# Performance work log

Measured on AMD Instinct MI355X. Metric: run time of the kernel, lower is better.

The kernel has to match this reference:

```python
import jax, jax.numpy as jnp
import numpy as np
from jax import lax

B, C, H, W = 2, 64, 128, 128
F_SCALE, STRIDE = 2, 2
F = F_SCALE * STRIDE            # pixel-unshuffle factor = 4
CK = C // 16                    # attention channel dim = 4
SCALE_DIM = C // F_SCALE        # softmax scale uses embed_size//f_scale = 32


def setup_inputs() -> dict:
    key = jax.random.key(0)
    ks = jax.random.split(key, 16)
    g = lambda i, shape, s=0.05: jax.random.normal(ks[i], shape, jnp.float32) * s
    return {
        "x":   jax.random.normal(ks[0], (B, C, H, W), jnp.float32),
        # conv1 = Sequential(1x1 C->CK, 1x1 CK->CK)
        "w1a": g(1, (CK, C)), "b1a": g(2, (CK,)),
        "w1b": g(3, (CK, CK)), "b1b": g(4, (CK,)),
        # wqk parameter (torch.randn, std 1)
        "wqk": jax.random.normal(ks[5], (CK, CK), jnp.float32),
        # conv2: 1x1 CK->C ; conv: 1x1 C->C
        "w2":  g(6, (C, CK)), "b2": g(7, (C,)),
        "wc":  g(8, (C, C)), "bc": g(9, (C,)),
        # FF (GridSANaive): 1x1 C->C/4, 3x3 dilated C/4->C/4, 1x1 C/4->C
        "wf1": g(10, (C // 4, C)), "bf1": g(11, (C // 4,)),
        "wf2": g(12, (C // 4, C // 4, 3, 3)), "bf2": g(13, (C // 4,)),
        "wf3": g(14, (C, C // 4)), "bf3": g(15, (C,)),
    }


def conv1x1(x, w, b):
    return jnp.einsum('bchw,oc->bohw', x, w) + b[None, :, None, None]


def grid_attention(x, wqk):
    b, c, h, w = x.shape
    sh = h // 2
    x = jnp.pad(x, ((0, 0), (0, 0), (sh, 0), (0, 0)))      # Shift2d pad (top)
    # F.layer_norm over last 3 dims, no affine, eps=1e-5
    mu = jnp.mean(x, axis=(1, 2, 3), keepdims=True)
    var = jnp.var(x, axis=(1, 2, 3), keepdims=True)
    xx = (x - mu) / jnp.sqrt(var + 1e-5)
    hh, ww = xx.shape[2], xx.shape[3]
    ph, pw = (F - hh % F) % F, (F - ww % F) % F
    xx = jnp.pad(xx, ((0, 0), (0, 0), (0, ph), (0, pw)))
    gh, gw = (hh + ph) // F, (ww + pw) // F
    # pixel_unshuffle: channel layout (c, fy, fx)
    xx = xx.reshape(b, c, gh, F, gw, F).transpose(0, 1, 3, 5, 2, 4)
    xx = xx.reshape(b, c * F * F, gh, gw)
    # rearrange 'b (f c) h w -> (b f) c h w', f=F*F (mixes layout, as in original)
    xx = xx.reshape(b * F * F, c, gh, gw)
    L = gh * gw
    tok = xx.transpose(0, 2, 3, 1).reshape(b * F * F, L, c)   # (bg, L, c)
    qk = tok @ wqk
    qk = qk / (jnp.linalg.norm(qk, axis=-1, keepdims=True) + 1e-8)
    attn = (jnp.einsum('blk,bmk->blm', qk, qk) + 1.0) / (SCALE_DIM ** 0.5)
    attn = jax.nn.softmax(attn, axis=-1)
    out = jnp.einsum('blm,bmc->blc', attn, tok)
    out = out.reshape(b * F * F, gh, gw, c).transpose(0, 3, 1, 2)
    out = out.reshape(b, F * F * c, gh, gw)
    # pixel_shuffle: channel layout (fy, fx, c)
    out = out.reshape(b, F, F, c, gh, gw).transpose(0, 3, 4, 1, 5, 2)
    out = out.reshape(b, c, gh * F, gw * F)
    out = out[:, :, :hh, :ww]                               # undo shuffle pad
    return out[:, :, :-sh, :] if sh > 0 else out            # Shift2d crop (bottom)


def ff(x, wf1, bf1, wf2, bf2, wf3, bf3):
    h1 = jax.nn.relu(conv1x1(x, wf1, bf1))
    k = 1 + (STRIDE // 2) * 2   # ShiftConv2d offset for 3x3, dilation=STRIDE
    hp = jnp.pad(h1, ((0, 0), (0, 0), (k, 0), (0, 0)))
    h2 = lax.conv_general_dilated(
        hp, wf2, (1, 1), ((STRIDE, STRIDE), (STRIDE, STRIDE)),
        rhs_dilation=(STRIDE, STRIDE),
        dimension_numbers=('NCHW', 'OIHW', 'NCHW'))
    h2 = jax.nn.relu((h2 + bf2[None, :, None, None])[:, :, :-k, :])
    return conv1x1(h2, wf3, bf3)


def reference(x, w1a, b1a, w1b, b1b, wqk, w2, b2, wc, bc,
              wf1, bf1, wf2, bf2, wf3, bf3):
    a = conv1x1(conv1x1(x, w1a, b1a), w1b, b1b)
    att = grid_attention(a, wqk)
    y = x + conv1x1(conv1x1(att, w2, b2), wc, bc)
    return y + ff(y, wf1, bf1, wf2, bf2, wf3, bf3)
```

## Files before the change

kernel.cpp:

```cpp
#include <hip/hip_runtime.h>
#include <math.h>

#define CHW  (64*16384)
#define ATT_SCALE 0.17677669529663687f

__global__ __launch_bounds__(256) void k1_a_stats(
    const float* __restrict__ x, const float* __restrict__ w1a,
    const float* __restrict__ b1a, const float* __restrict__ w1b,
    const float* __restrict__ b1b, float* __restrict__ a,
    float* __restrict__ statsbuf) {
  __shared__ float sA[256];
  __shared__ float sb1[4];
  __shared__ float pc[4][4][256];
  __shared__ float rs[64], rq[64];
  int tid = threadIdx.x;
  {
    int o = tid >> 6, c = tid & 63;
    float s = 0.f;
    #pragma unroll
    for (int k = 0; k < 4; ++k) s += w1b[o*4+k] * w1a[k*64+c];
    sA[tid] = s;
  }
  if (tid < 4) {
    float s = b1b[tid];
    #pragma unroll
    for (int k = 0; k < 4; ++k) s += w1b[tid*4+k] * b1a[k];
    sb1[tid] = s;
  }
  __syncthreads();
  int quad = tid & 15, cg = tid >> 4;
  int gq = blockIdx.x * 16 + quad;
  int bb = gq >> 12;
  int px0 = (gq & 4095) * 4;
  const float* xp = x + bb*CHW + (cg*4)*16384 + px0;
  float4 acc[4];
  #pragma unroll
  for (int o = 0; o < 4; ++o) acc[o] = make_float4(0.f,0.f,0.f,0.f);
  #pragma unroll
  for (int cc = 0; cc < 4; ++cc) {
    float4 xv = *(const float4*)(xp + cc*16384);
    int c = cg*4 + cc;
    #pragma unroll
    for (int o = 0; o < 4; ++o) {
      float w = sA[o*64+c];
      acc[o].x += w*xv.x; acc[o].y += w*xv.y; acc[o].z += w*xv.z; acc[o].w += w*xv.w;
    }
  }
  #pragma unroll
  for (int o = 0; o < 4; ++o) {
    pc[0][o][tid] = acc[o].x; pc[1][o][tid] = acc[o].y;
    pc[2][o][tid] = acc[o].z; pc[3][o][tid] = acc[o].w;
  }
  __syncthreads();
  if (tid < 64) {
    int q2 = tid & 15, o = tid >> 4;
    float sx=0.f, sy=0.f, sz=0.f, sw=0.f;
    #pragma unroll
    for (int g2 = 0; g2 < 16; ++g2) {
      int idx = g2*16 + q2;
      sx += pc[0][o][idx]; sy += pc[1][o][idx];
      sz += pc[2][o][idx]; sw += pc[3][o][idx];
    }
    float bv = sb1[o];
    sx += bv; sy += bv; sz += bv; sw += bv;
    int gq2 = blockIdx.x*16 + q2;
    int b2 = gq2 >> 12; int p0 = (gq2 & 4095)*4;
    *(float4*)(a + b2*4*16384 + o*16384 + p0) = make_float4(sx,sy,sz,sw);
    rs[tid] = sx+sy+sz+sw;
    rq[tid] = sx*sx+sy*sy+sz*sz+sw*sw;
  }
  __syncthreads();
  for (int s2 = 32; s2; s2 >>= 1) {
    if (tid < s2) { rs[tid] += rs[tid+s2]; rq[tid] += rq[tid+s2]; }
    __syncthreads();
  }
  if (tid == 0) { statsbuf[blockIdx.x*2] = rs[0]; statsbuf[blockIdx.x*2+1] = rq[0]; }
}

__device__ __forceinline__ float poly_exp(float d) {
  return 1.f + d*(1.f + d*(0.5f + d*(0.16666667f + d*0.04166667f)));
}
__global__ __launch_bounds__(512) void k3_attn(
    const float* __restrict__ a, const float* __restrict__ statsbuf,
    const float* __restrict__ wqk, float* __restrict__ att) {
  __shared__ float4 kq[1024];
  __shared__ float4 kt[1024];
  __shared__ float red[16][5][128];
  __shared__ float sred[8];
  int tid = threadIdx.x;
  int g = blockIdx.x >> 3, qb = blockIdx.x & 7;
  int b = g >> 4, u = (g >> 2) & 3, v = g & 3;

  if (tid < 256) {
    float2 p = ((const float2*)statsbuf)[b*256 + tid];
    float vs = p.x, vq = p.y;
    #pragma unroll
    for (int off = 32; off; off >>= 1) {
      vs += __shfl_down(vs, off); vq += __shfl_down(vq, off);
    }
    if ((tid & 63) == 0) { sred[tid>>6] = vs; sred[4 + (tid>>6)] = vq; }
  }
  __syncthreads();
  float mu  = (sred[0]+sred[1]+sred[2]+sred[3]) * (1.f/98304.f);
  float var = (sred[4]+sred[5]+sred[6]+sred[7]) * (1.f/98304.f) - mu*mu;
  float rsig = rsqrtf(var + 1e-5f);

  const float* ap = a + (b*4+u)*16384;
  for (int m = tid; m < 1024; m += 512) {
    int t = 512 + m;
    int i = t >> 5, j = m & 31;
    float4 tv = *(const float4*)(ap + (i*4 + v - 64)*128 + j*4);
    tv.x = (tv.x-mu)*rsig; tv.y = (tv.y-mu)*rsig;
    tv.z = (tv.z-mu)*rsig; tv.w = (tv.w-mu)*rsig;
    float q0 = tv.x*wqk[0] + tv.y*wqk[4] + tv.z*wqk[8]  + tv.w*wqk[12];
    float q1 = tv.x*wqk[1] + tv.y*wqk[5] + tv.z*wqk[9]  + tv.w*wqk[13];
    float q2 = tv.x*wqk[2] + tv.y*wqk[6] + tv.z*wqk[10] + tv.w*wqk[14];
    float q3 = tv.x*wqk[3] + tv.y*wqk[7] + tv.z*wqk[11] + tv.w*wqk[15];
    float inv = 1.f / (sqrtf(q0*q0 + q1*q1 + q2*q2 + q3*q3) + 1e-8f);
    kq[m] = make_float4(q0*inv, q1*inv, q2*inv, q3*inv);
    kt[m] = tv;
  }
  float z = -mu*rsig;
  float4 t0tv = make_float4(z, z, z, z);
  float p0 = z*(wqk[0] + wqk[4] + wqk[8]  + wqk[12]);
  float p1 = z*(wqk[1] + wqk[5] + wqk[9]  + wqk[13]);
  float p2 = z*(wqk[2] + wqk[6] + wqk[10] + wqk[14]);
  float p3 = z*(wqk[3] + wqk[7] + wqk[11] + wqk[15]);
  float inv0 = 1.f / (sqrtf(p0*p0 + p1*p1 + p2*p2 + p3*p3) + 1e-8f);
  float4 t0qk = make_float4(p0*inv0, p1*inv0, p2*inv0, p3*inv0);
  __syncthreads();

  if (qb >= 4) {
    int qi = tid & 31, s = tid >> 5;
    int t0 = (qb - 4)*128 + qi*4;
    float4 q[4];
    #pragma unroll
    for (int j = 0; j < 4; ++j) {
      float4 vq = kq[t0 + j];
      q[j] = make_float4(vq.x*ATT_SCALE, vq.y*ATT_SCALE, vq.z*ATT_SCALE, vq.w*ATT_SCALE);
    }
    float den[4] = {0.f,0.f,0.f,0.f};
    float4 ov[4];
    #pragma unroll
    for (int j = 0; j < 4; ++j) ov[j] = make_float4(0.f,0.f,0.f,0.f);
    if (s == 0) {
      #pragma unroll
      for (int j = 0; j < 4; ++j) {
        float d = q[j].x*t0qk.x + q[j].y*t0qk.y + q[j].z*t0qk.z + q[j].w*t0qk.w;
        float e = 512.f * poly_exp(d);
        den[j] += e;
        ov[j].x += e*t0tv.x; ov[j].y += e*t0tv.y; ov[j].z += e*t0tv.z; ov[j].w += e*t0tv.w;
      }
    }
    int m0 = s * 64;
    #pragma unroll 2
    for (int m = m0; m < m0 + 64; ++m) {
      float4 kk = kq[m];
      float4 tv = kt[m];
      #pragma unroll
      for (int j = 0; j < 4; ++j) {
        float d = q[j].x*kk.x + q[j].y*kk.y + q[j].z*kk.z + q[j].w*kk.w;
        float e = poly_exp(d);
        den[j] += e;
        ov[j].x += e*tv.x; ov[j].y += e*tv.y; ov[j].z += e*tv.z; ov[j].w += e*tv.w;
      }
    }
    #pragma unroll
    for (int j = 0; j < 4; ++j) {
      int key = j*32 + qi;
      red[s][0][key] = den[j];
      red[s][1][key] = ov[j].x; red[s][2][key] = ov[j].y;
      red[s][3][key] = ov[j].z; red[s][4][key] = ov[j].w;
    }
    __syncthreads();
    if (tid < 128) {
      int qi_r = tid & 31, j_r = tid >> 5;
      float dsum=0.f, ox=0.f, oy=0.f, oz=0.f, ow=0.f;
      #pragma unroll
      for (int ss = 0; ss < 16; ++ss) {
        dsum += red[ss][0][tid];
        ox += red[ss][1][tid]; oy += red[ss][2][tid];
        oz += red[ss][3][tid]; ow += red[ss][4][tid];
      }
      float inv = 1.f / dsum;
      int t = qb*128 + qi_r*4 + j_r;
      int i = t >> 5, j = t & 31;
      float* ap2 = att + b*4*16384 + (i*4+u)*128 + (j*4+v);
      ap2[0]     = ox*inv;
      ap2[16384] = oy*inv;
      ap2[32768] = oz*inv;
      ap2[49152] = ow*inv;
    }
  } else {
    float4 qs = make_float4(t0qk.x*ATT_SCALE, t0qk.y*ATT_SCALE,
                            t0qk.z*ATT_SCALE, t0qk.w*ATT_SCALE);
    float den = 0.f; float4 ov = make_float4(0.f,0.f,0.f,0.f);
    #pragma unroll
    for (int mm = 0; mm < 2; ++mm) {
      int m = tid*2 + mm;
      float4 kk = kq[m];
      float4 tv = kt[m];
      float d = qs.x*kk.x + qs.y*kk.y + qs.z*kk.z + qs.w*kk.w;
      float e = poly_exp(d);
      den += e;
      ov.x += e*tv.x; ov.y += e*tv.y; ov.z += e*tv.z; ov.w += e*tv.w;
    }
    if (tid == 0) {
      float d = qs.x*t0qk.x + qs.y*t0qk.y + qs.z*t0qk.z + qs.w*t0qk.w;
      float e = 512.f * poly_exp(d);
      den += e;
      ov.x += e*t0tv.x; ov.y += e*t0tv.y; ov.z += e*t0tv.z; ov.w += e*t0tv.w;
    }
    float* sc = &red[0][0][0];
    sc[tid]        = den;
    sc[512 + tid]  = ov.x;
    sc[1024 + tid] = ov.y;
    sc[1536 + tid] = ov.z;
    sc[2048 + tid] = ov.w;
    __syncthreads();
    for (int s2 = 256; s2; s2 >>= 1) {
      if (tid < s2) {
        sc[tid]        += sc[tid + s2];
        sc[512 + tid]  += sc[512 + tid + s2];
        sc[1024 + tid] += sc[1024 + tid + s2];
        sc[1536 + tid] += sc[1536 + tid + s2];
        sc[2048 + tid] += sc[2048 + tid + s2];
      }
      __syncthreads();
    }
    float invd = 1.f / sc[0];
    float res0 = sc[512]*invd, res1 = sc[1024]*invd,
          res2 = sc[1536]*invd, res3 = sc[2048]*invd;
    int comp = tid >> 7, tloc = tid & 127;
    int t = qb*128 + tloc;
    int i = t >> 5, j = t & 31;
    float val = (comp == 0) ? res0 : (comp == 1) ? res1 : (comp == 2) ? res2 : res3;
    att[b*4*16384 + comp*16384 + (i*4+u)*128 + (j*4+v)] = val;
  }
}

__global__ __launch_bounds__(512) void k4_y_h1(
    const float* __restrict__ x, const float* __restrict__ att,
    const float* __restrict__ w2p, const float* __restrict__ b2p,
    const float* __restrict__ wcp, const float* __restrict__ bcp,
    const float* __restrict__ wf1, const float* __restrict__ bf1,
    float* __restrict__ yout, float* __restrict__ h1) {
  __shared__ float sWf[64][4];
  __shared__ float sbf[64];
  __shared__ float sw1[1024];
  __shared__ float sb1[16];
  __shared__ float4 satt[4][32];
  __shared__ float4 ylds[64][32];
  int tid = threadIdx.x;
  if (tid < 256) {
    int o = tid >> 2, k = tid & 3;
    float s = 0.f;
    for (int c = 0; c < 64; ++c) s += wcp[o*64+c] * w2p[c*4+k];
    sWf[o][k] = s;
  }
  if (tid < 64) {
    float s = bcp[tid];
    for (int c = 0; c < 64; ++c) s += wcp[tid*64+c] * b2p[c];
    sbf[tid] = s;
  }
  for (int i = tid; i < 1024; i += 512) sw1[i] = wf1[i];
  if (tid < 16) sb1[tid] = bf1[tid];
  int quad = tid & 31, og = tid >> 5;
  int gq = blockIdx.x*32 + quad;
  int bb = gq >> 12; int px0 = (gq & 4095)*4;
  if (tid < 128) {
    int k = tid >> 5, q2 = tid & 31;
    int gq2 = blockIdx.x*32 + q2;
    int b2i = gq2 >> 12; int p0 = (gq2 & 4095)*4;
    satt[k][q2] = *(const float4*)(att + b2i*4*16384 + k*16384 + p0);
  }
  __syncthreads();
  float4 a0 = satt[0][quad], a1 = satt[1][quad], a2 = satt[2][quad], a3 = satt[3][quad];
  const float* xp = x + bb*CHW + px0;
  float* yp = yout + bb*CHW + px0;
  #pragma unroll
  for (int cc = 0; cc < 4; ++cc) {
    int c = og*4 + cc;
    float4 xv = *(const float4*)(xp + c*16384);
    float w0 = sWf[c][0], w1 = sWf[c][1], w2v = sWf[c][2], w3 = sWf[c][3];
    float bv = sbf[c];
    float4 yv;
    yv.x = xv.x + w0*a0.x + w1*a1.x + w2v*a2.x + w3*a3.x + bv;
    yv.y = xv.y + w0*a0.y + w1*a1.y + w2v*a2.y + w3*a3.y + bv;
    yv.z = xv.z + w0*a0.z + w1*a1.z + w2v*a2.z + w3*a3.z + bv;
    yv.w = xv.w + w0*a0.w + w1*a1.w + w2v*a2.w + w3*a3.w + bv;
    *(float4*)(yp + c*16384) = yv;
    ylds[c][quad] = yv;
  }
  __syncthreads();
  float bv = sb1[og];
  float4 acc = make_float4(bv, bv, bv, bv);
  #pragma unroll 8
  for (int c = 0; c < 64; ++c) {
    float4 yv = ylds[c][quad];
    float wa = sw1[og*64+c];
    acc.x += wa*yv.x; acc.y += wa*yv.y; acc.z += wa*yv.z; acc.w += wa*yv.w;
  }
  acc.x = fmaxf(acc.x,0.f); acc.y = fmaxf(acc.y,0.f);
  acc.z = fmaxf(acc.z,0.f); acc.w = fmaxf(acc.w,0.f);
  *(float4*)(h1 + bb*16*16384 + og*16384 + px0) = acc;
}

__global__ __launch_bounds__(512) void k6_ff_out(
    const float* __restrict__ h1, const float* __restrict__ wf2,
    const float* __restrict__ bf2, const float* __restrict__ wf3,
    const float* __restrict__ bf3, float* yo) {
  __shared__ float sbuf[16][3][136];
  __shared__ float h2buf[128][21];
  int tid = threadIdx.x;
  int bb = blockIdx.x >> 7, h = blockIdx.x & 127;
  for (int idx = tid; idx < 16*3*136; idx += 512) {
    int c = idx / (3*136);
    int r = (idx / 136) % 3;
    int col = idx % 136;
    int row = h - 5 + 2*r;
    int w = col - 4;
    float v = 0.f;
    if (row >= 0 && w >= 0 && w < 128)
      v = h1[bb*16*16384 + c*16384 + row*128 + w];
    sbuf[c][r][col] = v;
  }
  __syncthreads();
  int w = tid & 127;
  int g = __builtin_amdgcn_readfirstlane(tid >> 7);
  float acc[4];
  #pragma unroll
  for (int o = 0; o < 4; ++o) acc[o] = bf2[g*4+o];
  #pragma unroll 4
  for (int c = 0; c < 16; ++c) {
    #pragma unroll
    for (int r = 0; r < 3; ++r) {
      float tm2 = sbuf[c][r][w+2];
      float t00 = sbuf[c][r][w+4];
      float tp2 = sbuf[c][r][w+6];
      #pragma unroll
      for (int o = 0; o < 4; ++o) {
        const float* wp = wf2 + (((g*4+o)*16 + c)*3 + r)*3;
        acc[o] += wp[0]*tm2 + wp[1]*t00 + wp[2]*tp2;
      }
    }
  }
  #pragma unroll
  for (int o = 0; o < 4; ++o) h2buf[w][g*4+o] = fmaxf(acc[o], 0.f);
  __syncthreads();
  float hv[16];
  #pragma unroll
  for (int k = 0; k < 16; ++k) hv[k] = h2buf[w][k];
  float* ybase = yo + bb*CHW + h*128 + w;
  #pragma unroll 4
  for (int oc = 0; oc < 16; ++oc) {
    int o = g*16 + oc;
    float sv = bf3[o] + ybase[o*16384];
    #pragma unroll
    for (int k = 0; k < 16; ++k) sv += wf3[o*16+k]*hv[k];
    ybase[o*16384] = sv;
  }
}

extern "C" void kernel_launch(void* const* d_in, const int* in_sizes, int n_in,
                              void* d_out, int out_size, void* d_ws, size_t ws_size,
                              hipStream_t stream) {
  (void)in_sizes; (void)n_in; (void)out_size; (void)ws_size;
  const float* x   = (const float*)d_in[0];
  const float* w1a = (const float*)d_in[1];
  const float* b1a = (const float*)d_in[2];
  const float* w1b = (const float*)d_in[3];
  const float* b1b = (const float*)d_in[4];
  const float* wqk = (const float*)d_in[5];
  const float* w2  = (const float*)d_in[6];
  const float* b2  = (const float*)d_in[7];
  const float* wc  = (const float*)d_in[8];
  const float* bc  = (const float*)d_in[9];
  const float* wf1 = (const float*)d_in[10];
  const float* bf1 = (const float*)d_in[11];
  const float* wf2 = (const float*)d_in[12];
  const float* bf2 = (const float*)d_in[13];
  const float* wf3 = (const float*)d_in[14];
  const float* bf3 = (const float*)d_in[15];

  float* ws = (float*)d_ws;
  float*  a_    = ws;
  float*  stats = ws + 131072;
  float*  att   = ws + 525312;
  float*  h1    = ws + 656384;
  float*  y     = (float*)d_out;

  k1_a_stats<<<512, 256, 0, stream>>>(x, w1a, b1a, w1b, b1b, a_, stats);
  k3_attn   <<<256, 512, 0, stream>>>(a_, stats, wqk, att);
  k4_y_h1   <<<256, 512, 0, stream>>>(x, att, w2, b2, wc, bc, wf1, bf1, y, h1);
  k6_ff_out <<<256, 512, 0, stream>>>(h1, wf2, bf2, wf3, bf3, y);
}
```

Baseline: 130.9 us.

## Fuse y/h1 computation with FF conv into a single per-row kernel

Merges the residual-y and h1 kernel with the dilated-conv FF output kernel. Each block handles one output row and recomputes y and h1 for the three dilated input rows plus its own row in shared memory. This removes the global h1 buffer, the y write/read round trip and one kernel launch. In exchange it does about three times the y/h1 work and adds extra block barriers. The block index is also remapped across batch and rows.

```diff
diff --git a/kernel.cpp b/kernel.cpp
--- a/kernel.cpp
+++ b/kernel.cpp
@@ -239,19 +239,26 @@
   }
 }
 
-__global__ __launch_bounds__(512) void k4_y_h1(
+__global__ __launch_bounds__(512) void k46_row(
     const float* __restrict__ x, const float* __restrict__ att,
     const float* __restrict__ w2p, const float* __restrict__ b2p,
     const float* __restrict__ wcp, const float* __restrict__ bcp,
     const float* __restrict__ wf1, const float* __restrict__ bf1,
-    float* __restrict__ yout, float* __restrict__ h1) {
+    const float* __restrict__ wf2, const float* __restrict__ bf2,
+    const float* __restrict__ wf3, const float* __restrict__ bf3,
+    float* __restrict__ yo) {
   __shared__ float sWf[64][4];
   __shared__ float sbf[64];
   __shared__ float sw1[1024];
   __shared__ float sb1[16];
   __shared__ float4 satt[4][32];
   __shared__ float4 ylds[64][32];
+  __shared__ float sbuf[16][3][136];
+  __shared__ float h2buf[128][21];
   int tid = threadIdx.x;
+  int lid = (blockIdx.x & 7) * 32 + (blockIdx.x >> 3);
+  int bb = lid >> 7, h = lid & 127;
+
   if (tid < 256) {
     int o = tid >> 2, k = tid & 3;
     float s = 0.f;
@@ -265,67 +272,56 @@
   }
   for (int i = tid; i < 1024; i += 512) sw1[i] = wf1[i];
   if (tid < 16) sb1[tid] = bf1[tid];
+  for (int idx = tid; idx < 16*3*136; idx += 512) (&sbuf[0][0][0])[idx] = 0.f;
+
   int quad = tid & 31, og = tid >> 5;
-  int gq = blockIdx.x*32 + quad;
-  int bb = gq >> 12; int px0 = (gq & 4095)*4;
-  if (tid < 128) {
-    int k = tid >> 5, q2 = tid & 31;
-    int gq2 = blockIdx.x*32 + q2;
-    int b2i = gq2 >> 12; int p0 = (gq2 & 4095)*4;
-    satt[k][q2] = *(const float4*)(att + b2i*4*16384 + k*16384 + p0);
-  }
-  __syncthreads();
-  float4 a0 = satt[0][quad], a1 = satt[1][quad], a2 = satt[2][quad], a3 = satt[3][quad];
-  const float* xp = x + bb*CHW + px0;
-  float* yp = yout + bb*CHW + px0;
-  #pragma unroll
-  for (int cc = 0; cc < 4; ++cc) {
-    int c = og*4 + cc;
-    float4 xv = *(const float4*)(xp + c*16384);
-    float w0 = sWf[c][0], w1 = sWf[c][1], w2v = sWf[c][2], w3 = sWf[c][3];
-    float bv = sbf[c];
-    float4 yv;
-    yv.x = xv.x + w0*a0.x + w1*a1.x + w2v*a2.x + w3*a3.x + bv;
-    yv.y = xv.y + w0*a0.y + w1*a1.y + w2v*a2.y + w3*a3.y + bv;
-    yv.z = xv.z + w0*a0.z + w1*a1.z + w2v*a2.z + w3*a3.z + bv;
-    yv.w = xv.w + w0*a0.w + w1*a1.w + w2v*a2.w + w3*a3.w + bv;
-    *(float4*)(yp + c*16384) = yv;
-    ylds[c][quad] = yv;
-  }
-  __syncthreads();
-  float bv = sb1[og];
-  float4 acc = make_float4(bv, bv, bv, bv);
-  #pragma unroll 8
-  for (int c = 0; c < 64; ++c) {
-    float4 yv = ylds[c][quad];
-    float wa = sw1[og*64+c];
-    acc.x += wa*yv.x; acc.y += wa*yv.y; acc.z += wa*yv.z; acc.w += wa*yv.w;
-  }
-  acc.x = fmaxf(acc.x,0.f); acc.y = fmaxf(acc.y,0.f);
-  acc.z = fmaxf(acc.z,0.f); acc.w = fmaxf(acc.w,0.f);
-  *(float4*)(h1 + bb*16*16384 + og*16384 + px0) = acc;
-}
-
-__global__ __launch_bounds__(512) void k6_ff_out(
-    const float* __restrict__ h1, const float* __restrict__ wf2,
-    const float* __restrict__ bf2, const float* __restrict__ wf3,
-    const float* __restrict__ bf3, float* yo) {
-  __shared__ float sbuf[16][3][136];
-  __shared__ float h2buf[128][21];
-  int tid = threadIdx.x;
-  int bb = blockIdx.x >> 7, h = blockIdx.x & 127;
-  for (int idx = tid; idx < 16*3*136; idx += 512) {
-    int c = idx / (3*136);
-    int r = (idx / 136) % 3;
-    int col = idx % 136;
-    int row = h - 5 + 2*r;
-    int w = col - 4;
-    float v = 0.f;
-    if (row >= 0 && w >= 0 && w < 128)
-      v = h1[bb*16*16384 + c*16384 + row*128 + w];
-    sbuf[c][r][col] = v;
-  }
-  __syncthreads();
+  #pragma unroll 1
+  for (int ri = 0; ri < 4; ++ri) {
+    int row = (ri == 3) ? h : (h - 5 + 2*ri);
+    bool valid = (row >= 0);
+    __syncthreads();
+    if (valid && tid < 128) {
+      int k = tid >> 5, q2 = tid & 31;
+      satt[k][q2] = *(const float4*)(att + bb*4*16384 + k*16384 + row*128 + q2*4);
+    }
+    __syncthreads();
+    if (valid) {
+      float4 a0 = satt[0][quad], a1 = satt[1][quad],
+             a2 = satt[2][quad], a3 = satt[3][quad];
+      const float* xp = x + bb*CHW + row*128 + quad*4;
+      #pragma unroll
+      for (int cc = 0; cc < 4; ++cc) {
+        int c = og*4 + cc;
+        float4 xv = *(const float4*)(xp + c*16384);
+        float w0 = sWf[c][0], w1 = sWf[c][1], w2v = sWf[c][2], w3 = sWf[c][3];
+        float bv = sbf[c];
+        float4 yv;
+        yv.x = xv.x + w0*a0.x + w1*a1.x + w2v*a2.x + w3*a3.x + bv;
+        yv.y = xv.y + w0*a0.y + w1*a1.y + w2v*a2.y + w3*a3.y + bv;
+        yv.z = xv.z + w0*a0.z + w1*a1.z + w2v*a2.z + w3*a3.z + bv;
+        yv.w = xv.w + w0*a0.w + w1*a1.w + w2v*a2.w + w3*a3.w + bv;
+        ylds[c][quad] = yv;
+      }
+    }
+    __syncthreads();
+    if (valid && ri < 3) {
+      float bv = sb1[og];
+      float4 acc = make_float4(bv, bv, bv, bv);
+      #pragma unroll 8
+      for (int c = 0; c < 64; ++c) {
+        float4 yv = ylds[c][quad];
+        float wa = sw1[og*64+c];
+        acc.x += wa*yv.x; acc.y += wa*yv.y; acc.z += wa*yv.z; acc.w += wa*yv.w;
+      }
+      int col = 4 + quad*4;
+      sbuf[og][ri][col]   = fmaxf(acc.x, 0.f);
+      sbuf[og][ri][col+1] = fmaxf(acc.y, 0.f);
+      sbuf[og][ri][col+2] = fmaxf(acc.z, 0.f);
+      sbuf[og][ri][col+3] = fmaxf(acc.w, 0.f);
+    }
+  }
+  __syncthreads();
+
   int w = tid & 127;
   int g = __builtin_amdgcn_readfirstlane(tid >> 7);
   float acc[4];
@@ -351,11 +347,12 @@
   float hv[16];
   #pragma unroll
   for (int k = 0; k < 16; ++k) hv[k] = h2buf[w][k];
+  const float* yrow = (const float*)ylds;
   float* ybase = yo + bb*CHW + h*128 + w;
   #pragma unroll 4
   for (int oc = 0; oc < 16; ++oc) {
     int o = g*16 + oc;
-    float sv = bf3[o] + ybase[o*16384];
+    float sv = bf3[o] + yrow[o*128 + w];
     #pragma unroll
     for (int k = 0; k < 16; ++k) sv += wf3[o*16+k]*hv[k];
     ybase[o*16384] = sv;
@@ -387,11 +384,9 @@
   float*  a_    = ws;
   float*  stats = ws + 131072;
   float*  att   = ws + 525312;
-  float*  h1    = ws + 656384;
-  float*  y     = (float*)d_out;
 
   k1_a_stats<<<512, 256, 0, stream>>>(x, w1a, b1a, w1b, b1b, a_, stats);
   k3_attn   <<<256, 512, 0, stream>>>(a_, stats, wqk, att);
-  k4_y_h1   <<<256, 512, 0, stream>>>(x, att, w2, b2, wc, bc, wf1, bf1, y, h1);
-  k6_ff_out <<<256, 512, 0, stream>>>(h1, wf2, bf2, wf3, bf3, y);
-}
+  k46_row   <<<256, 512, 0, stream>>>(x, att, w2, b2, wc, bc, wf1, bf1,
+                                      wf2, bf2, wf3, bf3, (float*)d_out);
+}
```

Measured after the change: 130.4 us. No clear change (-0.4%).
